# Kernel optimization log

Hardware: AMD Instinct MI355X
Metric: run time of the kernel (lower is better)

The kernel has to match this reference:

```python
import math
import jax, jax.numpy as jnp
import numpy as np

N_KV = 8
GROUP = 4
HEAD_DIM = 128
BATCH = 512
CACHE = 2048
CONTEXT = 4096
NEG_INF = -10000.0


def setup_inputs() -> dict:
    key = jax.random.key(0)
    k = jax.random.split(key, 6)
    queries = jax.random.normal(k[0], (N_KV * GROUP, BATCH, HEAD_DIM), jnp.float32)
    keys = jax.random.normal(k[1], (N_KV, BATCH, HEAD_DIM), jnp.float32)
    key_t_caches = jax.random.normal(k[2], (N_KV, HEAD_DIM, CACHE), jnp.float32)
    values = jax.random.normal(k[3], (N_KV, BATCH, HEAD_DIM), jnp.float32)
    value_caches = jax.random.normal(k[4], (N_KV, CACHE, HEAD_DIM), jnp.float32)
    # causal bias: token b (global position CACHE+b) may attend to positions <= CACHE+b;
    # padded tail [CACHE+BATCH, CONTEXT) is always masked with NEG_INF
    pos = jnp.arange(CONTEXT)[None, :]                       # [1, CONTEXT]
    limit = (CACHE + jnp.arange(BATCH))[:, None]             # [BATCH, 1]
    attn_bias = jnp.where(pos <= limit, 0.0, NEG_INF).astype(jnp.float32)
    kq_scale = jnp.asarray([1.0 / math.sqrt(HEAD_DIM)], jnp.float32)
    return {
        "queries": queries,
        "keys": keys,
        "key_t_caches": key_t_caches,
        "values": values,
        "value_caches": value_caches,
        "attn_bias": attn_bias,
        "kq_scale": kq_scale,
    }


def reference(queries, keys, key_t_caches, values, value_caches, attn_bias, kq_scale):
    n_kv, B, D = keys.shape
    n_heads = queries.shape[0]
    group = n_heads // n_kv
    cache = key_t_caches.shape[-1]
    context = attn_bias.shape[-1]
    pad = context - cache - B

    scaled_keys = keys * kq_scale                            # [kv, B, D]
    scaled_values = jnp.maximum(values, NEG_INF)             # [kv, B, D]

    # pad new keys/values to fill context, then prepend cache (matches torch pad+cat)
    padded_kt = jnp.pad(scaled_keys.transpose(0, 2, 1), ((0, 0), (0, 0), (0, pad)))
    all_keys_t = jnp.concatenate([key_t_caches, padded_kt], axis=-1)   # [kv, D, context]
    padded_v = jnp.pad(scaled_values, ((0, 0), (0, pad), (0, 0)))
    all_values = jnp.concatenate([value_caches, padded_v], axis=1)     # [kv, context, D]

    q = queries.reshape(n_kv, group, B, D)                   # group-major per kv head
    scores = jnp.einsum('kgbd,kdc->kgbc', q, all_keys_t) + attn_bias   # [kv, g, B, context]
    probs = jax.nn.softmax(scores, axis=-1)
    out = jnp.einsum('kgbc,kcd->kgbd', probs, all_values)    # [kv, g, B, D]
    head_outs = out.reshape(n_heads, B, D)
    return head_outs, scaled_keys, scaled_values
```

## Files before the change

kernel.cpp:

```cpp
#include <hip/hip_runtime.h>
#include <hip/hip_bf16.h>

#define NKV 8
#define NHEADS 32
#define HDIM 128
#define BATCH 512
#define CACHE 2048
#define CTX_TOT 2560
#define CT 64
#define SPLITS 6
#define KPITCH 136
#define VPITCH 72
#define PPITCH 72
#define NEG_BIG (-1e30f)

typedef __attribute__((ext_vector_type(8))) _Float16 half8;
typedef __attribute__((ext_vector_type(4))) float floatx4;

__global__ __launch_bounds__(256) void prep(const float* __restrict__ ktc,
                                            const float* __restrict__ vc,
                                            const float* __restrict__ keys,
                                            const float* __restrict__ values,
                                            const float* __restrict__ kq,
                                            float* __restrict__ outk,
                                            float* __restrict__ outv,
                                            _Float16* __restrict__ Kh,
                                            _Float16* __restrict__ Vth) {
    __shared__ float tile[128 * 33];
    const int bid = blockIdx.x;
    const int t = threadIdx.x;

    if (bid < 512) {
        int c0 = (bid & 63) * 32, kv = bid >> 6;
        const float* src = ktc + (size_t)kv * HDIM * CACHE + c0;
#pragma unroll
        for (int i = 0; i < 4; i++) {
            int idx = t + 256 * i;
            int d = idx >> 3, cc = idx & 7;
            float4 v = *(const float4*)(src + (size_t)d * CACHE + cc * 4);
            *(float4*)(&tile[d * 33 + cc * 4]) = v;
        }
        __syncthreads();
        _Float16* dst = Kh + ((size_t)kv * CTX_TOT + c0) * HDIM;
#pragma unroll
        for (int i = 0; i < 2; i++) {
            int c = (t >> 4) + 16 * i, dg = t & 15;
            half8 o;
#pragma unroll
            for (int k = 0; k < 8; k++) o[k] = (_Float16)tile[(dg * 8 + k) * 33 + c];
            *(half8*)(dst + (size_t)c * HDIM + dg * 8) = o;
        }
    } else if (bid < 1024) {
        int l = bid - 512;
        int c1 = (l & 15) * 128, d0 = ((l >> 4) & 3) * 32, kv = l >> 6;
        const float* src = vc + ((size_t)kv * CACHE + c1) * HDIM + d0;
#pragma unroll
        for (int i = 0; i < 4; i++) {
            int idx = t + 256 * i;
            int c = idx >> 3, dc = idx & 7;
            float4 v = *(const float4*)(src + (size_t)c * HDIM + dc * 4);
            *(float4*)(&tile[c * 33 + dc * 4]) = v;
        }
        __syncthreads();
        _Float16* dst = Vth + ((size_t)kv * HDIM + d0) * CTX_TOT + c1;
#pragma unroll
        for (int i = 0; i < 2; i++) {
            int d = (t >> 4) + 16 * i, cg = t & 15;
            half8 o;
#pragma unroll
            for (int k = 0; k < 8; k++) o[k] = (_Float16)tile[(cg * 8 + k) * 33 + d];
            *(half8*)(dst + (size_t)d * CTX_TOT + cg * 8) = o;
        }
    } else if (bid < 1536) {
        int base = ((bid - 1024) * 256 + t) * 4;
        float s = kq[0];
        float4 v = *(const float4*)(keys + base);
        v.x *= s; v.y *= s; v.z *= s; v.w *= s;
        *(float4*)(outk + base) = v;
        int kv = base >> 16;
        int rem = base & 0xFFFF;
        _Float16* dst = Kh + ((size_t)kv * CTX_TOT + CACHE) * HDIM + rem;
        dst[0] = (_Float16)v.x; dst[1] = (_Float16)v.y;
        dst[2] = (_Float16)v.z; dst[3] = (_Float16)v.w;
    } else {
        int l = bid - 1536;
        int b1 = (l & 3) * 128, d0 = ((l >> 2) & 3) * 32, kv = l >> 4;
        const float* src = values + ((size_t)kv * BATCH + b1) * HDIM + d0;
        float* dst32 = outv + ((size_t)kv * BATCH + b1) * HDIM + d0;
#pragma unroll
        for (int i = 0; i < 4; i++) {
            int idx = t + 256 * i;
            int b = idx >> 3, dc = idx & 7;
            float4 v = *(const float4*)(src + (size_t)b * HDIM + dc * 4);
            v.x = fmaxf(v.x, -10000.0f); v.y = fmaxf(v.y, -10000.0f);
            v.z = fmaxf(v.z, -10000.0f); v.w = fmaxf(v.w, -10000.0f);
            *(float4*)(dst32 + (size_t)b * HDIM + dc * 4) = v;
            *(float4*)(&tile[b * 33 + dc * 4]) = v;
        }
        __syncthreads();
        _Float16* dst = Vth + ((size_t)kv * HDIM + d0) * CTX_TOT + CACHE + b1;
#pragma unroll
        for (int i = 0; i < 2; i++) {
            int d = (t >> 4) + 16 * i, bg = t & 15;
            half8 o;
#pragma unroll
            for (int k = 0; k < 8; k++) o[k] = (_Float16)tile[(bg * 8 + k) * 33 + d];
            *(half8*)(dst + (size_t)d * CTX_TOT + bg * 8) = o;
        }
    }
}

__global__ __launch_bounds__(256, 2) void attn_split(const float* __restrict__ q_g,
                                                     const _Float16* __restrict__ Kh,
                                                     const _Float16* __restrict__ Vth,
                                                     _Float16* __restrict__ Opart,
                                                     float* __restrict__ MLpart) {
    __shared__ _Float16 Klds[CT * KPITCH];
    __shared__ _Float16 Vlds[HDIM * VPITCH];
    __shared__ _Float16 Plds[4][32 * PPITCH];

    const int h = blockIdx.x & 31;
    const int qb2 = blockIdx.x >> 5;
    const int s = blockIdx.y;
    const int kv = h >> 2;
    const int t = threadIdx.x;
    const int wave = t >> 6;
    const int lane = t & 63;
    const int l15 = lane & 15, quad = lane >> 4;

    const float LOG2E = 1.44269504088896340736f;
    const int qrow0 = qb2 * 128 + wave * 16;

    half8 qfrag[2][4];
#pragma unroll
    for (int hh = 0; hh < 2; hh++) {
        const float* qp = q_g + ((size_t)h * BATCH + qrow0 + hh * 64 + l15) * HDIM + quad * 8;
#pragma unroll
        for (int kb = 0; kb < 4; kb++) {
            const float* p = qp + kb * 32;
            float4 a = *(const float4*)p;
            float4 b = *(const float4*)(p + 4);
            qfrag[hh][kb][0] = (_Float16)(a.x * LOG2E); qfrag[hh][kb][1] = (_Float16)(a.y * LOG2E);
            qfrag[hh][kb][2] = (_Float16)(a.z * LOG2E); qfrag[hh][kb][3] = (_Float16)(a.w * LOG2E);
            qfrag[hh][kb][4] = (_Float16)(b.x * LOG2E); qfrag[hh][kb][5] = (_Float16)(b.y * LOG2E);
            qfrag[hh][kb][6] = (_Float16)(b.z * LOG2E); qfrag[hh][kb][7] = (_Float16)(b.w * LOG2E);
        }
    }

    floatx4 O[2][8];
#pragma unroll
    for (int hh = 0; hh < 2; hh++)
#pragma unroll
        for (int nb = 0; nb < 8; nb++) O[hh][nb] = (floatx4){0.f, 0.f, 0.f, 0.f};
    float m_r[2][4], l_r[2][4];
#pragma unroll
    for (int hh = 0; hh < 2; hh++)
#pragma unroll
        for (int r = 0; r < 4; r++) { m_r[hh][r] = NEG_BIG; l_r[hh][r] = 0.f; }

    const int nT = 34 + 2 * qb2;

    for (int tt = s; tt < nT; tt += SPLITS) {
        const int c0 = tt * CT;
        __syncthreads();
#pragma unroll
        for (int i = 0; i < 4; i++) {
            int ch = t + 256 * i;
            int row = ch >> 4, j = ch & 15;
            uint4 v = *(const uint4*)(Kh + ((size_t)kv * CTX_TOT + c0 + row) * HDIM + j * 8);
            *(uint4*)(&Klds[row * KPITCH + j * 8]) = v;
        }
#pragma unroll
        for (int i = 0; i < 4; i++) {
            int ch = t + 256 * i;
            int row = ch >> 3, j = ch & 7;
            uint4 v = *(const uint4*)(Vth + ((size_t)kv * HDIM + row) * CTX_TOT + c0 + j * 8);
            *(uint4*)(&Vlds[row * VPITCH + j * 8]) = v;
        }
        __syncthreads();

        if (c0 <= CACHE + qrow0 + 64 + 15) {
            floatx4 S[2][4];
#pragma unroll
            for (int cs = 0; cs < 4; cs++) {
                floatx4 a0 = (floatx4){0.f, 0.f, 0.f, 0.f};
                floatx4 a1 = (floatx4){0.f, 0.f, 0.f, 0.f};
                int crow = cs * 16 + l15;
#pragma unroll
                for (int kb = 0; kb < 4; kb++) {
                    half8 kf = *(const half8*)(&Klds[crow * KPITCH + kb * 32 + quad * 8]);
                    a0 = __builtin_amdgcn_mfma_f32_16x16x32_f16(qfrag[0][kb], kf, a0, 0, 0, 0);
                    a1 = __builtin_amdgcn_mfma_f32_16x16x32_f16(qfrag[1][kb], kf, a1, 0, 0, 0);
                }
                S[0][cs] = a0; S[1][cs] = a1;
            }
#pragma unroll
            for (int hh = 0; hh < 2; hh++) {
                const int qr0h = qrow0 + hh * 64;
                if (c0 <= CACHE + qr0h + 15) {
                    if (c0 + CT > CACHE + qr0h) {
#pragma unroll
                        for (int cs = 0; cs < 4; cs++)
#pragma unroll
                            for (int r = 0; r < 4; r++) {
                                int c = c0 + cs * 16 + l15;
                                if (c > CACHE + qr0h + quad * 4 + r) S[hh][cs][r] = NEG_BIG;
                            }
                    }
                    float tmax[4];
#pragma unroll
                    for (int r = 0; r < 4; r++)
                        tmax[r] = fmaxf(fmaxf(S[hh][0][r], S[hh][1][r]),
                                        fmaxf(S[hh][2][r], S[hh][3][r]));
#pragma unroll
                    for (int off = 8; off >= 1; off >>= 1)
#pragma unroll
                        for (int r = 0; r < 4; r++)
                            tmax[r] = fmaxf(tmax[r], __shfl_xor(tmax[r], off, 64));
#pragma unroll
                    for (int r = 0; r < 4; r++) {
                        float mn = fmaxf(m_r[hh][r], tmax[r]);
                        float alpha = __builtin_amdgcn_exp2f(m_r[hh][r] - mn);
                        m_r[hh][r] = mn;
                        l_r[hh][r] *= alpha;
#pragma unroll
                        for (int nb = 0; nb < 8; nb++) O[hh][nb][r] *= alpha;
                    }
#pragma unroll
                    for (int cs = 0; cs < 4; cs++)
#pragma unroll
                        for (int r = 0; r < 4; r++) {
                            float p = __builtin_amdgcn_exp2f(S[hh][cs][r] - m_r[hh][r]);
                            l_r[hh][r] += p;
                            Plds[wave][(hh * 16 + quad * 4 + r) * PPITCH + cs * 16 + l15] = (_Float16)p;
                        }
                } else {
#pragma unroll
                    for (int cs = 0; cs < 4; cs++)
#pragma unroll
                        for (int r = 0; r < 4; r++)
                            Plds[wave][(hh * 16 + quad * 4 + r) * PPITCH + cs * 16 + l15] = (_Float16)0.f;
                }
            }
#pragma unroll
            for (int kb2 = 0; kb2 < 2; kb2++) {
                half8 pf0 = *(const half8*)(&Plds[wave][l15 * PPITCH + kb2 * 32 + quad * 8]);
                half8 pf1 = *(const half8*)(&Plds[wave][(16 + l15) * PPITCH + kb2 * 32 + quad * 8]);
#pragma unroll
                for (int nb = 0; nb < 8; nb++) {
                    half8 vf = *(const half8*)(&Vlds[(nb * 16 + l15) * VPITCH + kb2 * 32 + quad * 8]);
                    O[0][nb] = __builtin_amdgcn_mfma_f32_16x16x32_f16(pf0, vf, O[0][nb], 0, 0, 0);
                    O[1][nb] = __builtin_amdgcn_mfma_f32_16x16x32_f16(pf1, vf, O[1][nb], 0, 0, 0);
                }
            }
        }
    }

#pragma unroll
    for (int hh = 0; hh < 2; hh++)
#pragma unroll
        for (int off = 8; off >= 1; off >>= 1)
#pragma unroll
            for (int r = 0; r < 4; r++) l_r[hh][r] += __shfl_xor(l_r[hh][r], off, 64);

    const size_t rowbase = (size_t)s * NHEADS * BATCH + (size_t)h * BATCH;
#pragma unroll
    for (int hh = 0; hh < 2; hh++) {
#pragma unroll
        for (int nb = 0; nb < 8; nb++)
#pragma unroll
            for (int r = 0; r < 4; r++) {
                int brow = qrow0 + hh * 64 + quad * 4 + r;
                Opart[(rowbase + brow) * HDIM + nb * 16 + l15] = (_Float16)O[hh][nb][r];
            }
        if (l15 == 0) {
#pragma unroll
            for (int r = 0; r < 4; r++) {
                int brow = qrow0 + hh * 64 + quad * 4 + r;
                MLpart[(rowbase + brow) * 2 + 0] = m_r[hh][r];
                MLpart[(rowbase + brow) * 2 + 1] = l_r[hh][r];
            }
        }
    }
}

__global__ __launch_bounds__(256) void attn_merge(const _Float16* __restrict__ Opart,
                                                  const float* __restrict__ MLpart,
                                                  float* __restrict__ out) {
    const int t = threadIdx.x;
    const int row = blockIdx.x * 2 + (t >> 7);
    const int d = t & 127;
    const size_t stride = (size_t)NHEADS * BATCH;

    float m[SPLITS], l[SPLITS];
    float mm = NEG_BIG;
#pragma unroll
    for (int s = 0; s < SPLITS; s++) {
        m[s] = MLpart[((size_t)s * stride + row) * 2];
        l[s] = MLpart[((size_t)s * stride + row) * 2 + 1];
        mm = fmaxf(mm, m[s]);
    }
    float denom = 0.f, acc = 0.f;
#pragma unroll
    for (int s = 0; s < SPLITS; s++) {
        float w = __builtin_amdgcn_exp2f(m[s] - mm);
        denom += w * l[s];
        acc += w * (float)Opart[((size_t)s * stride + row) * HDIM + d];
    }
    out[(size_t)row * HDIM + d] = acc / denom;
}

extern "C" void kernel_launch(void* const* d_in, const int* in_sizes, int n_in,
                              void* d_out, int out_size, void* d_ws, size_t ws_size,
                              hipStream_t stream) {
    const float* queries = (const float*)d_in[0];
    const float* keys    = (const float*)d_in[1];
    const float* ktc     = (const float*)d_in[2];
    const float* values  = (const float*)d_in[3];
    const float* vcache  = (const float*)d_in[4];
    const float* kq      = (const float*)d_in[6];

    float* out     = (float*)d_out;
    float* out_sk  = out + (size_t)NHEADS * BATCH * HDIM;
    float* out_sv  = out_sk + (size_t)NKV * BATCH * HDIM;

    _Float16* Kh   = (_Float16*)d_ws;
    _Float16* Vth  = Kh + (size_t)NKV * CTX_TOT * HDIM;
    _Float16* Opart = Vth + (size_t)NKV * HDIM * CTX_TOT;
    float*    MLpart = (float*)(Opart + (size_t)SPLITS * NHEADS * BATCH * HDIM);

    prep<<<dim3(1664), dim3(256), 0, stream>>>(ktc, vcache, keys, values, kq,
                                               out_sk, out_sv, Kh, Vth);
    attn_split<<<dim3(128, SPLITS), dim3(256), 0, stream>>>(queries, Kh, Vth, Opart, MLpart);
    attn_merge<<<dim3(8192), dim3(256), 0, stream>>>(Opart, MLpart, out);
}
```

Baseline: 164.0 us.

## Load K/V fragments directly from global memory, drop LDS staging and barriers

Removes the shared-memory staging of K and V tiles and the two block-wide barriers per tile; each wave now reads its MFMA K and V fragments straight from global memory (relying on L1/L2 reuse across the four waves). The per-half causal skip checks are also removed, so every wave processes every tile in its range, and the number of context splits is raised from 6 to 8. This trades LDS traffic and synchronisation for more global/cache loads per wave and some extra masked compute, and raises grid size.

```diff
diff --git a/kernel.cpp b/kernel.cpp
--- a/kernel.cpp
+++ b/kernel.cpp
@@ -8,9 +8,7 @@
 #define CACHE 2048
 #define CTX_TOT 2560
 #define CT 64
-#define SPLITS 6
-#define KPITCH 136
-#define VPITCH 72
+#define SPLITS 8
 #define PPITCH 72
 #define NEG_BIG (-1e30f)
 
@@ -115,8 +113,6 @@
                                                      const _Float16* __restrict__ Vth,
                                                      _Float16* __restrict__ Opart,
                                                      float* __restrict__ MLpart) {
-    __shared__ _Float16 Klds[CT * KPITCH];
-    __shared__ _Float16 Vlds[HDIM * VPITCH];
     __shared__ _Float16 Plds[4][32 * PPITCH];
 
     const int h = blockIdx.x & 31;
@@ -131,6 +127,9 @@
     const float LOG2E = 1.44269504088896340736f;
     const int qrow0 = qb2 * 128 + wave * 16;
 
+    const _Float16* kg = Kh + (size_t)kv * CTX_TOT * HDIM;
+    const _Float16* vg = Vth + (size_t)kv * HDIM * CTX_TOT;
+
     half8 qfrag[2][4];
 #pragma unroll
     for (int hh = 0; hh < 2; hh++) {
@@ -162,96 +161,72 @@
 
     for (int tt = s; tt < nT; tt += SPLITS) {
         const int c0 = tt * CT;
-        __syncthreads();
-#pragma unroll
-        for (int i = 0; i < 4; i++) {
-            int ch = t + 256 * i;
-            int row = ch >> 4, j = ch & 15;
-            uint4 v = *(const uint4*)(Kh + ((size_t)kv * CTX_TOT + c0 + row) * HDIM + j * 8);
-            *(uint4*)(&Klds[row * KPITCH + j * 8]) = v;
-        }
-#pragma unroll
-        for (int i = 0; i < 4; i++) {
-            int ch = t + 256 * i;
-            int row = ch >> 3, j = ch & 7;
-            uint4 v = *(const uint4*)(Vth + ((size_t)kv * HDIM + row) * CTX_TOT + c0 + j * 8);
-            *(uint4*)(&Vlds[row * VPITCH + j * 8]) = v;
-        }
-        __syncthreads();
-
-        if (c0 <= CACHE + qrow0 + 64 + 15) {
-            floatx4 S[2][4];
-#pragma unroll
-            for (int cs = 0; cs < 4; cs++) {
-                floatx4 a0 = (floatx4){0.f, 0.f, 0.f, 0.f};
-                floatx4 a1 = (floatx4){0.f, 0.f, 0.f, 0.f};
-                int crow = cs * 16 + l15;
-#pragma unroll
-                for (int kb = 0; kb < 4; kb++) {
-                    half8 kf = *(const half8*)(&Klds[crow * KPITCH + kb * 32 + quad * 8]);
-                    a0 = __builtin_amdgcn_mfma_f32_16x16x32_f16(qfrag[0][kb], kf, a0, 0, 0, 0);
-                    a1 = __builtin_amdgcn_mfma_f32_16x16x32_f16(qfrag[1][kb], kf, a1, 0, 0, 0);
+
+        floatx4 S[2][4];
+#pragma unroll
+        for (int cs = 0; cs < 4; cs++) {
+            floatx4 a0 = (floatx4){0.f, 0.f, 0.f, 0.f};
+            floatx4 a1 = (floatx4){0.f, 0.f, 0.f, 0.f};
+            const _Float16* kr = kg + (size_t)(c0 + cs * 16 + l15) * HDIM + quad * 8;
+#pragma unroll
+            for (int kb = 0; kb < 4; kb++) {
+                half8 kf = *(const half8*)(kr + kb * 32);
+                a0 = __builtin_amdgcn_mfma_f32_16x16x32_f16(qfrag[0][kb], kf, a0, 0, 0, 0);
+                a1 = __builtin_amdgcn_mfma_f32_16x16x32_f16(qfrag[1][kb], kf, a1, 0, 0, 0);
+            }
+            S[0][cs] = a0; S[1][cs] = a1;
+        }
+        if (c0 + CT > CACHE + qrow0) {
+#pragma unroll
+            for (int hh = 0; hh < 2; hh++)
+#pragma unroll
+                for (int cs = 0; cs < 4; cs++)
+#pragma unroll
+                    for (int r = 0; r < 4; r++) {
+                        int c = c0 + cs * 16 + l15;
+                        if (c > CACHE + qrow0 + hh * 64 + quad * 4 + r) S[hh][cs][r] = NEG_BIG;
+                    }
+        }
+#pragma unroll
+        for (int hh = 0; hh < 2; hh++) {
+            float tmax[4];
+#pragma unroll
+            for (int r = 0; r < 4; r++)
+                tmax[r] = fmaxf(fmaxf(S[hh][0][r], S[hh][1][r]),
+                                fmaxf(S[hh][2][r], S[hh][3][r]));
+#pragma unroll
+            for (int off = 8; off >= 1; off >>= 1)
+#pragma unroll
+                for (int r = 0; r < 4; r++)
+                    tmax[r] = fmaxf(tmax[r], __shfl_xor(tmax[r], off, 64));
+#pragma unroll
+            for (int r = 0; r < 4; r++) {
+                float mn = fmaxf(m_r[hh][r], tmax[r]);
+                float alpha = __builtin_amdgcn_exp2f(m_r[hh][r] - mn);
+                m_r[hh][r] = mn;
+                l_r[hh][r] *= alpha;
+#pragma unroll
+                for (int nb = 0; nb < 8; nb++) O[hh][nb][r] *= alpha;
+            }
+#pragma unroll
+            for (int cs = 0; cs < 4; cs++)
+#pragma unroll
+                for (int r = 0; r < 4; r++) {
+                    float p = __builtin_amdgcn_exp2f(S[hh][cs][r] - m_r[hh][r]);
+                    l_r[hh][r] += p;
+                    Plds[wave][(hh * 16 + quad * 4 + r) * PPITCH + cs * 16 + l15] = (_Float16)p;
                 }
-                S[0][cs] = a0; S[1][cs] = a1;
-            }
-#pragma unroll
-            for (int hh = 0; hh < 2; hh++) {
-                const int qr0h = qrow0 + hh * 64;
-                if (c0 <= CACHE + qr0h + 15) {
-                    if (c0 + CT > CACHE + qr0h) {
-#pragma unroll
-                        for (int cs = 0; cs < 4; cs++)
-#pragma unroll
-                            for (int r = 0; r < 4; r++) {
-                                int c = c0 + cs * 16 + l15;
-                                if (c > CACHE + qr0h + quad * 4 + r) S[hh][cs][r] = NEG_BIG;
-                            }
-                    }
-                    float tmax[4];
-#pragma unroll
-                    for (int r = 0; r < 4; r++)
-                        tmax[r] = fmaxf(fmaxf(S[hh][0][r], S[hh][1][r]),
-                                        fmaxf(S[hh][2][r], S[hh][3][r]));
-#pragma unroll
-                    for (int off = 8; off >= 1; off >>= 1)
-#pragma unroll
-                        for (int r = 0; r < 4; r++)
-                            tmax[r] = fmaxf(tmax[r], __shfl_xor(tmax[r], off, 64));
-#pragma unroll
-                    for (int r = 0; r < 4; r++) {
-                        float mn = fmaxf(m_r[hh][r], tmax[r]);
-                        float alpha = __builtin_amdgcn_exp2f(m_r[hh][r] - mn);
-                        m_r[hh][r] = mn;
-                        l_r[hh][r] *= alpha;
-#pragma unroll
-                        for (int nb = 0; nb < 8; nb++) O[hh][nb][r] *= alpha;
-                    }
-#pragma unroll
-                    for (int cs = 0; cs < 4; cs++)
-#pragma unroll
-                        for (int r = 0; r < 4; r++) {
-                            float p = __builtin_amdgcn_exp2f(S[hh][cs][r] - m_r[hh][r]);
-                            l_r[hh][r] += p;
-                            Plds[wave][(hh * 16 + quad * 4 + r) * PPITCH + cs * 16 + l15] = (_Float16)p;
-                        }
-                } else {
-#pragma unroll
-                    for (int cs = 0; cs < 4; cs++)
-#pragma unroll
-                        for (int r = 0; r < 4; r++)
-                            Plds[wave][(hh * 16 + quad * 4 + r) * PPITCH + cs * 16 + l15] = (_Float16)0.f;
-                }
-            }
-#pragma unroll
-            for (int kb2 = 0; kb2 < 2; kb2++) {
-                half8 pf0 = *(const half8*)(&Plds[wave][l15 * PPITCH + kb2 * 32 + quad * 8]);
-                half8 pf1 = *(const half8*)(&Plds[wave][(16 + l15) * PPITCH + kb2 * 32 + quad * 8]);
-#pragma unroll
-                for (int nb = 0; nb < 8; nb++) {
-                    half8 vf = *(const half8*)(&Vlds[(nb * 16 + l15) * VPITCH + kb2 * 32 + quad * 8]);
-                    O[0][nb] = __builtin_amdgcn_mfma_f32_16x16x32_f16(pf0, vf, O[0][nb], 0, 0, 0);
-                    O[1][nb] = __builtin_amdgcn_mfma_f32_16x16x32_f16(pf1, vf, O[1][nb], 0, 0, 0);
-                }
+        }
+#pragma unroll
+        for (int kb2 = 0; kb2 < 2; kb2++) {
+            half8 pf0 = *(const half8*)(&Plds[wave][l15 * PPITCH + kb2 * 32 + quad * 8]);
+            half8 pf1 = *(const half8*)(&Plds[wave][(16 + l15) * PPITCH + kb2 * 32 + quad * 8]);
+#pragma unroll
+            for (int nb = 0; nb < 8; nb++) {
+                half8 vf = *(const half8*)(vg + (size_t)(nb * 16 + l15) * CTX_TOT
+                                              + c0 + kb2 * 32 + quad * 8);
+                O[0][nb] = __builtin_amdgcn_mfma_f32_16x16x32_f16(pf0, vf, O[0][nb], 0, 0, 0);
+                O[1][nb] = __builtin_amdgcn_mfma_f32_16x16x32_f16(pf1, vf, O[1][nb], 0, 0, 0);
             }
         }
     }
```

New measurement: 187.0 us. 1.14x slower.
